# Kernel optimization log

Measured on AMD Instinct MI355X. Metric: run time of the kernel, lower is better.

The kernel has to match this reference:

```python
import jax, jax.numpy as jnp
import numpy as np

CHANNEL = 512
INTER = CHANNEL // 2


def setup_inputs() -> dict:
    key = jax.random.key(0)
    k0, k1, k2, k3, k4 = jax.random.split(key, 5)
    b, c, h, w = 8, CHANNEL, 64, 64
    x = jax.random.normal(k0, (b, c, h, w), dtype=jnp.float32)
    # 1x1 conv weights, no bias: (out_ch, in_ch)
    s_in = 1.0 / np.sqrt(c)
    s_inter = 1.0 / np.sqrt(INTER)
    w_phi = jax.random.uniform(k1, (INTER, c), jnp.float32, -s_in, s_in)
    w_theta = jax.random.uniform(k2, (INTER, c), jnp.float32, -s_in, s_in)
    w_g = jax.random.uniform(k3, (INTER, c), jnp.float32, -s_in, s_in)
    w_mask = jax.random.uniform(k4, (c, INTER), jnp.float32, -s_inter, s_inter)
    return {"x": x, "w_phi": w_phi, "w_theta": w_theta, "w_g": w_g, "w_mask": w_mask}


def reference(x, w_phi, w_theta, w_g, w_mask):
    b, c, h, w = x.shape
    inter = c // 2
    # NOTE: original torch code views the (b, inter, h, w) conv outputs as
    # (b, c, -1), so n = h*w // 2 and the matmul 'feature' dim is the full c.
    n = (h * w) // 2
    phi = jnp.einsum('oc,bchw->bohw', w_phi, x).reshape(b, c, n)        # (b, c, n)
    theta = jnp.einsum('oc,bchw->bohw', w_theta, x).reshape(b, c, n)
    theta = jnp.transpose(theta, (0, 2, 1))                              # (b, n, c)
    g = jnp.einsum('oc,bchw->bohw', w_g, x).reshape(b, c, n)
    g = jnp.transpose(g, (0, 2, 1))                                      # (b, n, c)
    attn = jnp.matmul(theta, phi)                                        # (b, n, n)
    attn = jax.nn.softmax(attn, axis=1)                                  # softmax over dim=1 (columns)
    y = jnp.matmul(attn, g)                                              # (b, n, c)
    y = jnp.transpose(y, (0, 2, 1)).reshape(b, inter, h, w)              # (b, inter, h, w)
    mask = jnp.einsum('oc,bchw->bohw', w_mask, y)                        # (b, c, h, w)
    return mask + x
```

## Files before the change

### kernel.cpp

```cpp
#include <hip/hip_runtime.h>
#include <cstdint>
#include <cstddef>

typedef __attribute__((ext_vector_type(8))) _Float16 half8;
typedef __attribute__((ext_vector_type(8))) short short8;
typedef __attribute__((ext_vector_type(4))) float floatx4;

static __device__ __forceinline__ uint16_t f2h(float f) {
    _Float16 h = (_Float16)f;
    uint16_t u;
    __builtin_memcpy(&u, &h, 2);
    return u;
}
static __device__ __forceinline__ float h2f(uint16_t u) {
    _Float16 h;
    __builtin_memcpy(&h, &u, 2);
    return (float)h;
}
static __device__ __forceinline__ uint16_t f2bf(float f) {
    uint32_t u;
    __builtin_memcpy(&u, &f, 4);
    u += 0x7fffu + ((u >> 16) & 1u);
    return (uint16_t)(u >> 16);
}

static __device__ __forceinline__ void g2lds16(const void* g, void* l) {
    __builtin_amdgcn_global_load_lds((__attribute__((address_space(1))) void*)g,
                                     (__attribute__((address_space(3))) void*)l, 16, 0, 0);
}

__global__ void cvt_weights(const float* __restrict__ wphi, const float* __restrict__ wtheta,
                            const float* __restrict__ wg, const float* __restrict__ wmask,
                            uint16_t* __restrict__ W3, uint16_t* __restrict__ Wm, float* __restrict__ L) {
    int seg = blockIdx.y;
    int i = blockIdx.x * 256 + threadIdx.x;
    if (seg == 4) {
        if (i < 16384) L[i] = 0.f;
        return;
    }
    const float* src = seg == 0 ? wphi : seg == 1 ? wtheta : seg == 2 ? wg : wmask;
    uint16_t* dst = seg < 3 ? W3 + seg * 131072 : Wm;
    int base = i * 4;
    float4 v = *(const float4*)(src + base);
    *(ushort4*)(dst + base) = make_ushort4(f2h(v.x), f2h(v.y), f2h(v.z), f2h(v.w));
}

__global__ __launch_bounds__(256) void transpose_x(const float* __restrict__ x, uint16_t* __restrict__ xt) {
    __shared__ uint16_t tile[64][66];
    int b = blockIdx.z, p0 = blockIdx.x * 64, c0 = blockIdx.y * 64;
    int t0 = threadIdx.x & 63, t1 = threadIdx.x >> 6;
    const float* xb = x + ((long)b * 512 + c0) * 4096 + p0;
#pragma unroll
    for (int r = 0; r < 16; ++r) {
        int cc = t1 * 16 + r;
        tile[cc][t0] = f2h(xb[(long)cc * 4096 + t0]);
    }
    __syncthreads();
    uint16_t* xtb = xt + ((long)b * 4096 + p0) * 512 + c0;
#pragma unroll
    for (int r = 0; r < 16; ++r) {
        int pp = t1 * 16 + r;
        xtb[(long)pp * 512 + t0] = tile[t0][pp];
    }
}

__global__ void scale_g(uint16_t* __restrict__ gc, const float* __restrict__ L) {
    long t = (long)blockIdx.x * 256 + threadIdx.x;
    long base = t * 8;
    int j0 = (int)(base & 2047);
    int b = (int)(base >> 20);
    const float* Lp = L + (long)b * 2048 + j0;
    float4 l0 = *(const float4*)Lp;
    float4 l1 = *(const float4*)(Lp + 4);
    float rr[8] = {1.f / l0.x, 1.f / l0.y, 1.f / l0.z, 1.f / l0.w, 1.f / l1.x, 1.f / l1.y, 1.f / l1.z, 1.f / l1.w};
    uint4 v = *(uint4*)(gc + base);
    uint32_t* pv = (uint32_t*)&v;
    uint32_t o[4];
#pragma unroll
    for (int e = 0; e < 4; ++e) {
        float a = h2f((uint16_t)(pv[e] & 0xffffu)) * rr[2 * e];
        float c = h2f((uint16_t)(pv[e] >> 16)) * rr[2 * e + 1];
        o[e] = (uint32_t)f2bf(a) | ((uint32_t)f2bf(c) << 16);
    }
    *(uint4*)(gc + base) = *(uint4*)o;
}

template <bool KHALF, int EPI, bool SWAP, int BMODE, int DT>
__global__ __launch_bounds__(256) void gemm_nt(const uint16_t* __restrict__ A, const uint16_t* __restrict__ B,
                                               void* __restrict__ Cout, const float* __restrict__ resid,
                                               int lda, int ldb, int ldc, int nK,
                                               long aBatch, long bBatch, long cBatch,
                                               void* __restrict__ Cout2, int ldc2, long c2Batch,
                                               float* __restrict__ Lsum) {
    __shared__ uint16_t Al[2 * 128 * 32];
    __shared__ uint16_t Bl[2 * 128 * 32];
    const int b = blockIdx.z;
    const uint16_t* Ab = A + (long)b * aBatch;
    const uint16_t* Bb = B + (long)b * bBatch;
    const int m0 = (SWAP ? blockIdx.y : blockIdx.x) * 128;
    const int n0 = (SWAP ? blockIdx.x : blockIdx.y) * 128;
    const int tid = threadIdx.x;
    const int lane = tid & 63, wave = tid >> 6;
    const int ln = lane & 15, q = lane >> 4;
    const int wm = (wave & 1) * 64, wn = (wave >> 1) * 64;

    const float ainit = (EPI == 4) ? -12.f : 0.f;
    floatx4 acc[4][4];
#pragma unroll
    for (int i = 0; i < 4; ++i)
#pragma unroll
        for (int j = 0; j < 4; ++j) acc[i][j] = (floatx4){ainit, ainit, ainit, ainit};

    for (int kt = 0; kt < nK; ++kt) {
        int k0 = kt * 64;
#pragma unroll
        for (int half = 0; half < 2; ++half) {
            int kh = k0 + half * 32;
            int keff = kh;
            long roff = 0;
            if (KHALF && kh >= 256) { keff = kh - 256; roff = 2048; }
            uint16_t* AlH = &Al[half * 4096];
            uint16_t* BlH = &Bl[half * 4096];
#pragma unroll
            for (int s = 0; s < 2; ++s) {
                int c = tid + s * 256;
                int row = c >> 2, kq = (c & 3) * 8;
                g2lds16(Ab + ((long)(m0 + row) + roff) * lda + keff + kq, &AlH[c * 8]);
                if (BMODE == 0) {
                    g2lds16(Bb + ((long)(n0 + row) + roff) * ldb + keff + kq, &BlH[c * 8]);
                } else {
                    int pg = n0 + row;
                    int ii = pg & 2047, hh = pg >> 11;
                    const uint16_t* src = Bb + (long)ii * 512 + 2 * (keff + kq);
                    uint4 v0 = *(const uint4*)src;
                    uint4 v1 = *(const uint4*)(src + 8);
                    uint32_t* a = (uint32_t*)&v0;
                    uint32_t* cc = (uint32_t*)&v1;
                    uint32_t o[4];
                    if (hh == 0) {
                        o[0] = (a[0] & 0xffffu) | (a[1] << 16);
                        o[1] = (a[2] & 0xffffu) | (a[3] << 16);
                        o[2] = (cc[0] & 0xffffu) | (cc[1] << 16);
                        o[3] = (cc[2] & 0xffffu) | (cc[3] << 16);
                    } else {
                        o[0] = (a[0] >> 16) | (a[1] & 0xffff0000u);
                        o[1] = (a[2] >> 16) | (a[3] & 0xffff0000u);
                        o[2] = (cc[0] >> 16) | (cc[1] & 0xffff0000u);
                        o[3] = (cc[2] >> 16) | (cc[3] & 0xffff0000u);
                    }
                    *(uint4*)&BlH[c * 8] = *(uint4*)o;
                }
            }
        }
        __syncthreads();
#pragma unroll
        for (int half = 0; half < 2; ++half) {
            const uint16_t* AlH = &Al[half * 4096];
            const uint16_t* BlH = &Bl[half * 4096];
            short8 af[4], bfr[4];
#pragma unroll
            for (int mt = 0; mt < 4; ++mt) af[mt] = *(const short8*)&AlH[(wm + mt * 16 + ln) * 32 + q * 8];
#pragma unroll
            for (int nt = 0; nt < 4; ++nt) bfr[nt] = *(const short8*)&BlH[(wn + nt * 16 + ln) * 32 + q * 8];
#pragma unroll
            for (int mt = 0; mt < 4; ++mt)
#pragma unroll
                for (int nt = 0; nt < 4; ++nt) {
                    if constexpr (DT == 0) {
                        half8 ah, bh;
                        __builtin_memcpy(&ah, &af[mt], 16);
                        __builtin_memcpy(&bh, &bfr[nt], 16);
                        acc[mt][nt] = __builtin_amdgcn_mfma_f32_16x16x32_f16(ah, bh, acc[mt][nt], 0, 0, 0);
                    } else {
                        acc[mt][nt] = __builtin_amdgcn_mfma_f32_16x16x32_bf16(af[mt], bfr[nt], acc[mt][nt], 0, 0, 0);
                    }
                }
        }
        __syncthreads();
    }

    if (EPI == 0 || (EPI == 3 && n0 < 512)) {
        uint16_t* C = (uint16_t*)Cout + (long)b * cBatch;
#pragma unroll
        for (int mt = 0; mt < 4; ++mt)
#pragma unroll
            for (int r = 0; r < 4; ++r) {
                int gm = m0 + wm + mt * 16 + q * 4 + r;
#pragma unroll
                for (int nt = 0; nt < 4; ++nt) {
                    int gn = n0 + wn + nt * 16 + ln;
                    C[(long)gm * ldc + gn] = f2h(acc[mt][nt][r]);
                }
            }
    } else if (EPI == 4) {
        uint16_t* C = (uint16_t*)Cout + (long)b * cBatch;
        const int cb = n0 + wn + (ln << 2);
        float cs[4] = {0.f, 0.f, 0.f, 0.f};
#pragma unroll
        for (int mt = 0; mt < 4; ++mt)
#pragma unroll
            for (int r = 0; r < 4; ++r) {
                int gm = m0 + wm + mt * 16 + q * 4 + r;
                float e0 = __expf(acc[mt][0][r]);
                float e1 = __expf(acc[mt][1][r]);
                float e2 = __expf(acc[mt][2][r]);
                float e3 = __expf(acc[mt][3][r]);
                cs[0] += e0; cs[1] += e1; cs[2] += e2; cs[3] += e3;
                uint2 wv;
                wv.x = (uint32_t)f2bf(e0) | ((uint32_t)f2bf(e1) << 16);
                wv.y = (uint32_t)f2bf(e2) | ((uint32_t)f2bf(e3) << 16);
                *(uint2*)&C[(long)gm * ldc + cb] = wv;
            }
        cs[0] += __shfl_xor(cs[0], 16); cs[0] += __shfl_xor(cs[0], 32);
        cs[1] += __shfl_xor(cs[1], 16); cs[1] += __shfl_xor(cs[1], 32);
        cs[2] += __shfl_xor(cs[2], 16); cs[2] += __shfl_xor(cs[2], 32);
        cs[3] += __shfl_xor(cs[3], 16); cs[3] += __shfl_xor(cs[3], 32);
        {
            int srcl = lane >> 2;
            float t0 = __shfl(cs[0], srcl);
            float t1 = __shfl(cs[1], srcl);
            float t2 = __shfl(cs[2], srcl);
            float t3 = __shfl(cs[3], srcl);
            int sel = lane & 3;
            float val = sel == 0 ? t0 : sel == 1 ? t1 : sel == 2 ? t2 : t3;
            atomicAdd(&Lsum[(long)b * 2048 + n0 + wn + lane], val);
        }
    } else if (EPI == 1) {
        float* C = (float*)Cout + (long)b * cBatch;
        const float* X = resid + (long)b * cBatch;
#pragma unroll
        for (int mt = 0; mt < 4; ++mt)
#pragma unroll
            for (int r = 0; r < 4; ++r) {
                int gm = m0 + wm + mt * 16 + q * 4 + r;
#pragma unroll
                for (int nt = 0; nt < 4; ++nt) {
                    int gn = n0 + wn + nt * 16 + ln;
                    long idx = (long)gm * ldc + gn;
                    C[idx] = acc[mt][nt][r] + X[idx];
                }
            }
    } else {
        uint16_t* C = (uint16_t*)Cout2 + (long)b * c2Batch;
        const int cb = m0 + wm + q * 16;
#pragma unroll
        for (int nt = 0; nt < 4; ++nt) {
            int gn2 = n0 - 512 + wn + nt * 16 + ln;
            uint16_t* rowp = C + (long)gn2 * ldc2 + cb;
#pragma unroll
            for (int r = 0; r < 4; ++r) {
                ushort4 u = make_ushort4(f2h(acc[0][nt][r]), f2h(acc[1][nt][r]),
                                         f2h(acc[2][nt][r]), f2h(acc[3][nt][r]));
                *(ushort4*)&rowp[r * 4] = u;
            }
        }
    }
}

extern "C" void kernel_launch(void* const* d_in, const int* in_sizes, int n_in, void* d_out, int out_size, void* d_ws,
                              size_t ws_size, hipStream_t stream) {
    const float* x = (const float*)d_in[0];
    const float* wphi = (const float*)d_in[1];
    const float* wtheta = (const float*)d_in[2];
    const float* wg = (const float*)d_in[3];
    const float* wmask = (const float*)d_in[4];
    float* out = (float*)d_out;
    char* ws = (char*)d_ws;

    uint16_t* W3 = (uint16_t*)(ws + 0);
    uint16_t* Wm = (uint16_t*)(ws + 786432);
    float* L = (float*)(ws + 1048576);
    char* A_region = ws + 1179648;
    char* B_region = ws + 68288512;
    uint16_t* Xt = (uint16_t*)A_region;
    uint16_t* P = (uint16_t*)A_region;
    uint16_t* C2 = (uint16_t*)B_region;
    uint16_t* Y2 = (uint16_t*)B_region;
    uint16_t* Gc = (uint16_t*)(B_region + 33554432);

    cvt_weights<<<dim3(128, 5), 256, 0, stream>>>(wphi, wtheta, wg, wmask, W3, Wm, L);

    transpose_x<<<dim3(64, 8, 8), 256, 0, stream>>>(x, Xt);

    gemm_nt<false, 3, false, 0, 0><<<dim3(32, 6, 8), 256, 0, stream>>>(
        Xt, W3, C2, nullptr, 512, 512, 512, 8, 4096L * 512, 0, 4096L * 512, Gc, 4096, 256L * 4096, nullptr);

    gemm_nt<true, 4, false, 0, 0><<<dim3(16, 16, 8), 256, 0, stream>>>(
        C2 + 256, C2, P, nullptr, 512, 512, 2048, 8, 4096L * 512, 4096L * 512, 2048L * 2048, nullptr, 0, 0, L);

    scale_g<<<4096, 256, 0, stream>>>(Gc, L);

    gemm_nt<false, 0, true, 0, 1><<<dim3(4, 16, 8), 256, 0, stream>>>(
        P, Gc, Y2, nullptr, 2048, 2048, 512, 32, 2048L * 2048, 1048576L, 2048L * 512, nullptr, 0, 0, nullptr);

    gemm_nt<false, 1, false, 1, 0><<<dim3(4, 32, 8), 256, 0, stream>>>(
        Wm, Y2, out, x, 256, 512, 4096, 4, 0, 1048576L, 512L * 4096, nullptr, 0, 0, nullptr);
}
```

Baseline: 306.9 us.

## Permute mask weights and B-operand layouts so GEMM loads go direct to LDS

The mask weight matrix is now stored in a column-permuted order during conversion. The Y2 layout seen by the final GEMM is changed to match, so that GEMM's B operand loads straight to LDS with async global_load_lds. Before, it used register loads followed by 16-bit shuffles to de-interleave. The EPI 0 epilogue now writes packed ushort4 stores instead of scalar halves, and the attention-times-G GEMM uses a new B addressing mode. This removes VALU shuffle work and uncoalesced stores, but depends on the permuted layouts staying consistent across kernels.

```diff
diff --git a/kernel.cpp b/kernel.cpp
--- a/kernel.cpp
+++ b/kernel.cpp
@@ -38,11 +38,17 @@
         if (i < 16384) L[i] = 0.f;
         return;
     }
-    const float* src = seg == 0 ? wphi : seg == 1 ? wtheta : seg == 2 ? wg : wmask;
-    uint16_t* dst = seg < 3 ? W3 + seg * 131072 : Wm;
     int base = i * 4;
+    if (seg == 3) {
+        int row = base >> 8, dc = base & 255;
+        int blk = dc & 192, a = (dc >> 2) & 15;
+        const float* s = wmask + row * 256 + blk + a;
+        *(ushort4*)(Wm + base) = make_ushort4(f2h(s[0]), f2h(s[16]), f2h(s[32]), f2h(s[48]));
+        return;
+    }
+    const float* src = seg == 0 ? wphi : seg == 1 ? wtheta : wg;
     float4 v = *(const float4*)(src + base);
-    *(ushort4*)(dst + base) = make_ushort4(f2h(v.x), f2h(v.y), f2h(v.z), f2h(v.w));
+    *(ushort4*)(W3 + seg * 131072 + base) = make_ushort4(f2h(v.x), f2h(v.y), f2h(v.z), f2h(v.w));
 }
 
 __global__ __launch_bounds__(256) void transpose_x(const float* __restrict__ x, uint16_t* __restrict__ xt) {
@@ -128,27 +134,12 @@
                 g2lds16(Ab + ((long)(m0 + row) + roff) * lda + keff + kq, &AlH[c * 8]);
                 if (BMODE == 0) {
                     g2lds16(Bb + ((long)(n0 + row) + roff) * ldb + keff + kq, &BlH[c * 8]);
+                } else if (BMODE == 2) {
+                    int pg = n0 + row;
+                    g2lds16(Bb + (long)(pg & 2047) * ldb + ((pg >> 11) << 8) + keff + kq, &BlH[c * 8]);
                 } else {
-                    int pg = n0 + row;
-                    int ii = pg & 2047, hh = pg >> 11;
-                    const uint16_t* src = Bb + (long)ii * 512 + 2 * (keff + kq);
-                    uint4 v0 = *(const uint4*)src;
-                    uint4 v1 = *(const uint4*)(src + 8);
-                    uint32_t* a = (uint32_t*)&v0;
-                    uint32_t* cc = (uint32_t*)&v1;
-                    uint32_t o[4];
-                    if (hh == 0) {
-                        o[0] = (a[0] & 0xffffu) | (a[1] << 16);
-                        o[1] = (a[2] & 0xffffu) | (a[3] << 16);
-                        o[2] = (cc[0] & 0xffffu) | (cc[1] << 16);
-                        o[3] = (cc[2] & 0xffffu) | (cc[3] << 16);
-                    } else {
-                        o[0] = (a[0] >> 16) | (a[1] & 0xffff0000u);
-                        o[1] = (a[2] >> 16) | (a[3] & 0xffff0000u);
-                        o[2] = (cc[0] >> 16) | (cc[1] & 0xffff0000u);
-                        o[3] = (cc[2] >> 16) | (cc[3] & 0xffff0000u);
-                    }
-                    *(uint4*)&BlH[c * 8] = *(uint4*)o;
+                    int pr = n0 + row;
+                    g2lds16(Bb + (long)(pr & 255) * 4096 + ((pr >> 8) << 11) + keff + kq, &BlH[c * 8]);
                 }
             }
         }
@@ -179,7 +170,19 @@
         __syncthreads();
     }
 
-    if (EPI == 0 || (EPI == 3 && n0 < 512)) {
+    if (EPI == 0) {
+        uint16_t* C = (uint16_t*)Cout + (long)b * cBatch;
+        const int cb = n0 + wn + (ln << 2);
+#pragma unroll
+        for (int mt = 0; mt < 4; ++mt)
+#pragma unroll
+            for (int r = 0; r < 4; ++r) {
+                int gm = m0 + wm + mt * 16 + q * 4 + r;
+                ushort4 u = make_ushort4(f2h(acc[mt][0][r]), f2h(acc[mt][1][r]),
+                                         f2h(acc[mt][2][r]), f2h(acc[mt][3][r]));
+                *(ushort4*)&C[(long)gm * ldc + cb] = u;
+            }
+    } else if (EPI == 3 && n0 < 512) {
         uint16_t* C = (uint16_t*)Cout + (long)b * cBatch;
 #pragma unroll
         for (int mt = 0; mt < 4; ++mt)
@@ -290,9 +293,9 @@
 
     scale_g<<<4096, 256, 0, stream>>>(Gc, L);
 
-    gemm_nt<false, 0, true, 0, 1><<<dim3(4, 16, 8), 256, 0, stream>>>(
+    gemm_nt<false, 0, true, 3, 1><<<dim3(4, 16, 8), 256, 0, stream>>>(
         P, Gc, Y2, nullptr, 2048, 2048, 512, 32, 2048L * 2048, 1048576L, 2048L * 512, nullptr, 0, 0, nullptr);
 
-    gemm_nt<false, 1, false, 1, 0><<<dim3(4, 32, 8), 256, 0, stream>>>(
+    gemm_nt<false, 1, false, 2, 0><<<dim3(4, 32, 8), 256, 0, stream>>>(
         Wm, Y2, out, x, 256, 512, 4096, 4, 0, 1048576L, 512L * 4096, nullptr, 0, 0, nullptr);
 }
```

Result: faster. 297.8 us (-3.0%).
